# Kernel tuning notes

Hardware: AMD Instinct MI355X
Metric: run time of the kernel (lower is better)

Reference implementation:

```python
import jax, jax.numpy as jnp
import numpy as np

B, T, D, H = 4, 2048, 1024, 16
HD = D // H
EPS = 1e-5
NEG = 1e10


def setup_inputs() -> dict:
    key = jax.random.key(0)
    k1, k2, k3 = jax.random.split(key, 3)
    return {
        "target": jax.random.normal(k1, (B, T, D), dtype=jnp.float32),
        "w_qkv": jax.random.normal(k2, (D, 3 * D), dtype=jnp.float32) * 0.02,
        "w_proj": jax.random.normal(k3, (D, D), dtype=jnp.float32) * (0.02 / np.sqrt(24.0)),
        "b_proj": jnp.zeros((D,), dtype=jnp.float32),
        "ln_gamma": jnp.ones((D,), dtype=jnp.float32),
        "ln_beta": jnp.zeros((D,), dtype=jnp.float32),
    }


def reference(target, w_qkv, w_proj, b_proj, ln_gamma, ln_beta):
    b, t, d = target.shape
    resid = target
    qkv = target @ w_qkv                      # [B,T,3D]
    q, k, v = jnp.split(qkv, 3, axis=-1)
    # [B,H,T,hd]
    q = q.reshape(b, t, H, HD).transpose(0, 2, 1, 3)
    k = k.reshape(b, t, H, HD).transpose(0, 2, 1, 3)
    v = v.reshape(b, t, H, HD).transpose(0, 2, 1, 3)
    scores = jnp.einsum("bhqd,bhkd->bhqk", q, k) * (1.0 / np.sqrt(HD))
    causal = (jnp.arange(t)[:, None] >= jnp.arange(t)[None, :]).astype(scores.dtype)
    scores = scores * causal - (1.0 - causal) * NEG
    attn = jax.nn.softmax(scores, axis=-1)
    out = jnp.einsum("bhqk,bhkd->bhqd", attn, v)
    out = out.transpose(0, 2, 1, 3).reshape(b, t, d)
    proj = out @ w_proj + b_proj
    x = proj + resid
    mu = jnp.mean(x, axis=-1, keepdims=True)
    var = jnp.var(x, axis=-1, keepdims=True)
    return ((x - mu) * jax.lax.rsqrt(var + EPS)) * ln_gamma + ln_beta
```

## Files before the change

### kernel.cpp

```cpp
#include <hip/hip_runtime.h>
#include <hip/hip_bf16.h>

#define Bsz 4
#define Tseq 2048
#define Dmodel 1024
#define Hn 16
#define HD 64
#define EPS 1e-5f
#define QSCALE 0.18033688011112042f

typedef __attribute__((ext_vector_type(8))) short bf16x8;
typedef __attribute__((ext_vector_type(4))) float f32x4;
typedef __attribute__((ext_vector_type(4))) unsigned short us4;

typedef const __attribute__((address_space(1))) void* gas_t;
typedef __attribute__((address_space(3))) void* las_t;

__device__ __forceinline__ unsigned short f2bf(float x) {
    unsigned u = __builtin_bit_cast(unsigned, x);
    u += 0x7fffu + ((u >> 16) & 1u);
    return (unsigned short)(u >> 16);
}
__device__ __forceinline__ unsigned pack2bf_t(float a, float b) {
    return (__builtin_bit_cast(unsigned, a) >> 16)
         | (__builtin_bit_cast(unsigned, b) & 0xffff0000u);
}

__global__ void cast_bf16(const float* __restrict__ in, unsigned short* __restrict__ out) {
    int i = (blockIdx.x * 256 + threadIdx.x) * 4;
    float4 v = *(const float4*)(in + i);
    us4 o = { f2bf(v.x), f2bf(v.y), f2bf(v.z), f2bf(v.w) };
    *(us4*)(out + i) = o;
}

__global__ void transpose_cast(const float* __restrict__ in, unsigned short* __restrict__ out,
                               int K, int N) {
    __shared__ unsigned short t[32][33];
    int k0 = blockIdx.y * 32, n0 = blockIdx.x * 32;
    int tx = threadIdx.x, ty = threadIdx.y;
    #pragma unroll
    for (int i = 0; i < 32; i += 8)
        t[ty + i][tx] = f2bf(in[(size_t)(k0 + ty + i) * N + n0 + tx]);
    __syncthreads();
    #pragma unroll
    for (int i = 0; i < 32; i += 8)
        out[(size_t)(n0 + ty + i) * K + k0 + tx] = t[tx][ty + i];
}

template<bool OUT_BF16, bool SCALEQ>
__global__ __launch_bounds__(256)
void gemm_mfma(const unsigned short* __restrict__ A,
               const unsigned short* __restrict__ Bt,
               void* __restrict__ Cv, int M, int N, int K,
               const float* __restrict__ bias, const float* __restrict__ resid) {
    __shared__ unsigned short As[128 * 32];
    __shared__ unsigned short Bs[128 * 32];
    const int tid = threadIdx.x;
    const int w = tid >> 6, lane = tid & 63;
    const int l16 = lane & 15, quad = lane >> 4;
    const int m0 = blockIdx.y * 128, n0 = blockIdx.x * 128;

    f32x4 acc[4][4];
    #pragma unroll
    for (int i = 0; i < 4; ++i)
        #pragma unroll
        for (int j = 0; j < 4; ++j)
            acc[i][j] = f32x4{0.f, 0.f, 0.f, 0.f};

    const int lrow = lane >> 2, lcol = lane & 3;
    const unsigned short* ag = A  + (size_t)(m0 + w * 32 + lrow) * K + lcol * 8;
    const unsigned short* bg = Bt + (size_t)(n0 + w * 32 + lrow) * K + lcol * 8;
    unsigned short* al0 = As + (w * 32) * 32;
    unsigned short* al1 = As + (w * 32 + 16) * 32;
    unsigned short* bl0 = Bs + (w * 32) * 32;
    unsigned short* bl1 = Bs + (w * 32 + 16) * 32;
    const int am = (w >> 1) * 64, bn = (w & 1) * 64;

    for (int k0 = 0; k0 < K; k0 += 32) {
        __builtin_amdgcn_global_load_lds((gas_t)(ag + k0),          (las_t)al0, 16, 0, 0);
        __builtin_amdgcn_global_load_lds((gas_t)(ag + 16 * K + k0), (las_t)al1, 16, 0, 0);
        __builtin_amdgcn_global_load_lds((gas_t)(bg + k0),          (las_t)bl0, 16, 0, 0);
        __builtin_amdgcn_global_load_lds((gas_t)(bg + 16 * K + k0), (las_t)bl1, 16, 0, 0);
        __syncthreads();

        bf16x8 af[4], bf[4];
        #pragma unroll
        for (int i = 0; i < 4; ++i)
            af[i] = *(const bf16x8*)&As[(am + i * 16 + l16) * 32 + quad * 8];
        #pragma unroll
        for (int j = 0; j < 4; ++j)
            bf[j] = *(const bf16x8*)&Bs[(bn + j * 16 + l16) * 32 + quad * 8];
        #pragma unroll
        for (int i = 0; i < 4; ++i)
            #pragma unroll
            for (int j = 0; j < 4; ++j)
                acc[i][j] = __builtin_amdgcn_mfma_f32_16x16x32_bf16(af[i], bf[j], acc[i][j], 0, 0, 0);
        __syncthreads();
    }

    #pragma unroll
    for (int i = 0; i < 4; ++i) {
        #pragma unroll
        for (int j = 0; j < 4; ++j) {
            const int col = n0 + bn + j * 16 + l16;
            const float scale = (SCALEQ && col < Dmodel) ? QSCALE : 1.0f;
            #pragma unroll
            for (int r = 0; r < 4; ++r) {
                const int row = m0 + am + i * 16 + quad * 4 + r;
                if (OUT_BF16) {
                    ((unsigned short*)Cv)[(size_t)row * N + col] = f2bf(acc[i][j][r] * scale);
                } else {
                    float v = acc[i][j][r] + bias[col] + resid[(size_t)row * N + col];
                    ((float*)Cv)[(size_t)row * N + col] = v;
                }
            }
        }
    }
}

__global__ __launch_bounds__(256)
void flash_attn(const unsigned short* __restrict__ qkv, unsigned short* __restrict__ out) {
    const int x = blockIdx.x;
    const int qt_lo = x, qt_hi = (Tseq / 64 - 1) - x;
    const int bh = blockIdx.y;
    const int h = bh & (Hn - 1), b = bh >> 4;
    const int tid = threadIdx.x;
    const int wave = tid >> 6;
    const int lane = tid & 63;
    const int l16 = lane & 15;
    const int quad = lane >> 4;

    __shared__ unsigned short Ks[2][64 * 32];
    __shared__ unsigned short Vs[64 * 64];
    __shared__ unsigned short Ps[4][16 * 72];

    const unsigned short* qrow = qkv + ((size_t)(b * Tseq + wave * 16 + l16)) * 3072 + h * HD;
    const unsigned short* qhi = qrow + (size_t)qt_hi * 64 * 3072;
    const unsigned short* qlo = qrow + (size_t)qt_lo * 64 * 3072;
    bf16x8 qh0 = *(const bf16x8*)(qhi + quad * 8);
    bf16x8 qh1 = *(const bf16x8*)(qhi + 32 + quad * 8);
    bf16x8 ql0 = *(const bf16x8*)(qlo + quad * 8);
    bf16x8 ql1 = *(const bf16x8*)(qlo + 32 + quad * 8);

    float l_hi = 0.f, l_lo = 0.f;
    f32x4 ohi[4], olo[4];
    #pragma unroll
    for (int nt = 0; nt < 4; ++nt) {
        ohi[nt] = f32x4{0.f, 0.f, 0.f, 0.f};
        olo[nt] = f32x4{0.f, 0.f, 0.f, 0.f};
    }

    const unsigned short* kbase = qkv + (size_t)b * Tseq * 3072 + Dmodel + h * HD;
    const unsigned short* vbase = kbase + Dmodel;
    const unsigned short* kg = kbase + (size_t)(wave * 16 + (lane >> 2)) * 3072 + (lane & 3) * 8;
    unsigned short* kl0 = &Ks[0][wave * 16 * 32];
    unsigned short* kl1 = &Ks[1][wave * 16 * 32];
    const int vp = tid >> 3, vc = tid & 7;
    unsigned short* pw = Ps[wave];

    auto compute = [&](int q0t, const bf16x8& qf0, const bf16x8& qf1,
                       f32x4* oacc, float& l_part, bool diag, int k0g) {
        f32x4 st[4];
        #pragma unroll
        for (int nt = 0; nt < 4; ++nt) {
            f32x4 a = {0.f, 0.f, 0.f, 0.f};
            bf16x8 kf0 = *(const bf16x8*)&Ks[0][(nt * 16 + l16) * 32 + quad * 8];
            a = __builtin_amdgcn_mfma_f32_16x16x32_bf16(kf0, qf0, a, 0, 0, 0);
            bf16x8 kf1 = *(const bf16x8*)&Ks[1][(nt * 16 + l16) * 32 + quad * 8];
            a = __builtin_amdgcn_mfma_f32_16x16x32_bf16(kf1, qf1, a, 0, 0, 0);
            st[nt] = a;
        }
        if (diag) {
            const int qg = q0t + wave * 16 + l16;
            #pragma unroll
            for (int nt = 0; nt < 4; ++nt) {
                const int kgl = k0g + nt * 16 + quad * 4;
                #pragma unroll
                for (int r = 0; r < 4; ++r)
                    if (kgl + r > qg) st[nt][r] = -1e30f;
            }
        }
        float p[4][4];
        #pragma unroll
        for (int nt = 0; nt < 4; ++nt)
            #pragma unroll
            for (int r = 0; r < 4; ++r) {
                p[nt][r] = exp2f(st[nt][r]);
                l_part += p[nt][r];
            }
        #pragma unroll
        for (int nt = 0; nt < 4; ++nt) {
            unsigned* dst = (unsigned*)&pw[l16 * 72 + nt * 16 + quad * 4];
            dst[0] = pack2bf_t(p[nt][0], p[nt][1]);
            dst[1] = pack2bf_t(p[nt][2], p[nt][3]);
        }
        #pragma unroll
        for (int c = 0; c < 2; ++c) {
            bf16x8 pf = *(const bf16x8*)&pw[l16 * 72 + c * 32 + quad * 8];
            #pragma unroll
            for (int nt = 0; nt < 4; ++nt) {
                const int d = nt * 16 + l16;
                const int pc = (c * 4 + quad) ^ ((d + (d >> 3)) & 7);
                bf16x8 vf = *(const bf16x8*)&Vs[d * 64 + pc * 8];
                oacc[nt] = __builtin_amdgcn_mfma_f32_16x16x32_bf16(pf, vf, oacc[nt], 0, 0, 0);
            }
        }
    };

    for (int kt = 0; kt <= qt_hi; ++kt) {
        const size_t koff = (size_t)kt * 64 * 3072;
        __builtin_amdgcn_global_load_lds((gas_t)(kg + koff),      (las_t)kl0, 16, 0, 0);
        __builtin_amdgcn_global_load_lds((gas_t)(kg + koff + 32), (las_t)kl1, 16, 0, 0);
        {
            const unsigned short* vrow = vbase + koff + (size_t)(2 * vp) * 3072 + vc * 8;
            bf16x8 va = *(const bf16x8*)(vrow);
            bf16x8 vb = *(const bf16x8*)(vrow + 3072);
            const int kc = vp >> 2;
            const int kin = (2 * vp) & 7;
            #pragma unroll
            for (int j = 0; j < 8; ++j) {
                const int d = vc * 8 + j;
                const int pc = kc ^ ((d + (d >> 3)) & 7);
                unsigned pk = (unsigned)(unsigned short)va[j]
                            | ((unsigned)(unsigned short)vb[j] << 16);
                *(unsigned*)&Vs[d * 64 + pc * 8 + kin] = pk;
            }
        }
        __syncthreads();

        compute(qt_hi * 64, qh0, qh1, ohi, l_hi, kt == qt_hi, kt * 64);
        if (kt <= qt_lo)
            compute(qt_lo * 64, ql0, ql1, olo, l_lo, kt == qt_lo, kt * 64);
        __syncthreads();
    }

    auto epilogue = [&](int q0t, f32x4* oacc, float l_part) {
        l_part += __shfl_xor(l_part, 16, 64);
        l_part += __shfl_xor(l_part, 32, 64);
        float inv[4];
        #pragma unroll
        for (int r = 0; r < 4; ++r) {
            float lr = __shfl(l_part, quad * 4 + r, 64);
            inv[r] = __builtin_amdgcn_rcpf(lr);
        }
        unsigned short* obase =
            out + ((size_t)(b * Tseq + q0t + wave * 16)) * Dmodel + h * HD;
        #pragma unroll
        for (int nt = 0; nt < 4; ++nt) {
            #pragma unroll
            for (int r = 0; r < 4; ++r) {
                int row = quad * 4 + r;
                obase[(size_t)row * Dmodel + nt * 16 + l16] = f2bf(oacc[nt][r] * inv[r]);
            }
        }
    };
    epilogue(qt_hi * 64, ohi, l_hi);
    epilogue(qt_lo * 64, olo, l_lo);
}

__global__ void ln_kernel(float* __restrict__ x, const float* __restrict__ gamma,
                          const float* __restrict__ beta) {
    const int row = blockIdx.x;
    float* xr = x + (size_t)row * Dmodel;
    const int tid = threadIdx.x;
    __shared__ float rs[256], rs2[256];

    float4 v = *(const float4*)(xr + tid * 4);
    float s  = v.x + v.y + v.z + v.w;
    float s2 = v.x * v.x + v.y * v.y + v.z * v.z + v.w * v.w;
    rs[tid] = s; rs2[tid] = s2;
    __syncthreads();
    for (int off = 128; off; off >>= 1) {
        if (tid < off) { rs[tid] += rs[tid + off]; rs2[tid] += rs2[tid + off]; }
        __syncthreads();
    }
    const float mu  = rs[0] * (1.0f / Dmodel);
    const float var = rs2[0] * (1.0f / Dmodel) - mu * mu;
    const float rstd = rsqrtf(var + EPS);

    float4 g = *(const float4*)(gamma + tid * 4);
    float4 bt = *(const float4*)(beta + tid * 4);
    float4 o;
    o.x = (v.x - mu) * rstd * g.x + bt.x;
    o.y = (v.y - mu) * rstd * g.y + bt.y;
    o.z = (v.z - mu) * rstd * g.z + bt.z;
    o.w = (v.w - mu) * rstd * g.w + bt.w;
    *(float4*)(xr + tid * 4) = o;
}

extern "C" void kernel_launch(void* const* d_in, const int* in_sizes, int n_in,
                              void* d_out, int out_size, void* d_ws, size_t ws_size,
                              hipStream_t stream) {
    const float* target   = (const float*)d_in[0];
    const float* w_qkv    = (const float*)d_in[1];
    const float* w_proj   = (const float*)d_in[2];
    const float* b_proj   = (const float*)d_in[3];
    const float* ln_gamma = (const float*)d_in[4];
    const float* ln_beta  = (const float*)d_in[5];
    float* out = (float*)d_out;

    const int M = Bsz * Tseq;

    char* ws = (char*)d_ws;
    unsigned short* qkv_bf16 = (unsigned short*)(ws);
    unsigned short* attn_bf  = (unsigned short*)(ws + 48ull * 1024 * 1024);
    unsigned short* tgt_bf   = (unsigned short*)(ws + 64ull * 1024 * 1024);
    unsigned short* wqT      = (unsigned short*)(ws + 80ull * 1024 * 1024);
    unsigned short* wpT      = (unsigned short*)(ws + 86ull * 1024 * 1024);

    cast_bf16<<<dim3(M * Dmodel / 1024), 256, 0, stream>>>(target, tgt_bf);
    transpose_cast<<<dim3(3072 / 32, Dmodel / 32), dim3(32, 8), 0, stream>>>(
        w_qkv, wqT, Dmodel, 3072);
    transpose_cast<<<dim3(Dmodel / 32, Dmodel / 32), dim3(32, 8), 0, stream>>>(
        w_proj, wpT, Dmodel, Dmodel);

    gemm_mfma<true, true><<<dim3(3072 / 128, M / 128), 256, 0, stream>>>(
        tgt_bf, wqT, qkv_bf16, M, 3072, Dmodel, nullptr, nullptr);

    flash_attn<<<dim3(Tseq / 128, Bsz * Hn), 256, 0, stream>>>(qkv_bf16, attn_bf);

    gemm_mfma<false, false><<<dim3(Dmodel / 128, M / 128), 256, 0, stream>>>(
        attn_bf, wpT, out, M, Dmodel, Dmodel, b_proj, target);

    ln_kernel<<<dim3(M), 256, 0, stream>>>(out, ln_gamma, ln_beta);
}
```

Baseline: 322.2 us.

## Double-buffer V in LDS, load K fragments directly to registers, prefetch next V

Removes the K staging in shared memory. Each wave now loads its K MFMA fragments straight from global memory into registers, and every wave redundantly loads the full K tile. V is double-buffered in LDS: the next tile is loaded into registers during the current compute and written to the other buffer afterwards, which cuts one barrier per iteration. It also raises wave priority around the MFMA sections with s_setprio. The trade-off is four times more global/L2 traffic for K, uncoalesced 16-byte row loads, and higher register pressure from holding kf[8] plus the prefetched V.

```diff
diff --git a/kernel.cpp b/kernel.cpp
--- a/kernel.cpp
+++ b/kernel.cpp
@@ -130,8 +130,7 @@
     const int l16 = lane & 15;
     const int quad = lane >> 4;
 
-    __shared__ unsigned short Ks[2][64 * 32];
-    __shared__ unsigned short Vs[64 * 64];
+    __shared__ unsigned short Vs[2][64 * 64];
     __shared__ unsigned short Ps[4][16 * 72];
 
     const unsigned short* qrow = qkv + ((size_t)(b * Tseq + wave * 16 + l16)) * 3072 + h * HD;
@@ -152,22 +151,33 @@
 
     const unsigned short* kbase = qkv + (size_t)b * Tseq * 3072 + Dmodel + h * HD;
     const unsigned short* vbase = kbase + Dmodel;
-    const unsigned short* kg = kbase + (size_t)(wave * 16 + (lane >> 2)) * 3072 + (lane & 3) * 8;
-    unsigned short* kl0 = &Ks[0][wave * 16 * 32];
-    unsigned short* kl1 = &Ks[1][wave * 16 * 32];
+    const unsigned short* kfrag = kbase + (size_t)l16 * 3072 + quad * 8;
     const int vp = tid >> 3, vc = tid & 7;
+    const unsigned short* vsrc = vbase + (size_t)(2 * vp) * 3072 + vc * 8;
     unsigned short* pw = Ps[wave];
 
-    auto compute = [&](int q0t, const bf16x8& qf0, const bf16x8& qf1,
-                       f32x4* oacc, float& l_part, bool diag, int k0g) {
+    auto writeV = [&](int buf, const bf16x8& va, const bf16x8& vb) {
+        const int kc = vp >> 2;
+        const int kin = (2 * vp) & 7;
+        #pragma unroll
+        for (int j = 0; j < 8; ++j) {
+            const int d = vc * 8 + j;
+            const int pc = kc ^ ((d + (d >> 3)) & 7);
+            unsigned pk = (unsigned)(unsigned short)va[j]
+                        | ((unsigned)(unsigned short)vb[j] << 16);
+            *(unsigned*)&Vs[buf][d * 64 + pc * 8 + kin] = pk;
+        }
+    };
+
+    auto compute = [&](const bf16x8* kf, int q0t, const bf16x8& qf0, const bf16x8& qf1,
+                       f32x4* oacc, float& l_part, bool diag, int k0g, int vbuf) {
+        __builtin_amdgcn_s_setprio(1);
         f32x4 st[4];
         #pragma unroll
         for (int nt = 0; nt < 4; ++nt) {
             f32x4 a = {0.f, 0.f, 0.f, 0.f};
-            bf16x8 kf0 = *(const bf16x8*)&Ks[0][(nt * 16 + l16) * 32 + quad * 8];
-            a = __builtin_amdgcn_mfma_f32_16x16x32_bf16(kf0, qf0, a, 0, 0, 0);
-            bf16x8 kf1 = *(const bf16x8*)&Ks[1][(nt * 16 + l16) * 32 + quad * 8];
-            a = __builtin_amdgcn_mfma_f32_16x16x32_bf16(kf1, qf1, a, 0, 0, 0);
+            a = __builtin_amdgcn_mfma_f32_16x16x32_bf16(kf[2 * nt],     qf0, a, 0, 0, 0);
+            a = __builtin_amdgcn_mfma_f32_16x16x32_bf16(kf[2 * nt + 1], qf1, a, 0, 0, 0);
             st[nt] = a;
         }
         if (diag) {
@@ -201,37 +211,41 @@
             for (int nt = 0; nt < 4; ++nt) {
                 const int d = nt * 16 + l16;
                 const int pc = (c * 4 + quad) ^ ((d + (d >> 3)) & 7);
-                bf16x8 vf = *(const bf16x8*)&Vs[d * 64 + pc * 8];
+                bf16x8 vf = *(const bf16x8*)&Vs[vbuf][d * 64 + pc * 8];
                 oacc[nt] = __builtin_amdgcn_mfma_f32_16x16x32_bf16(pf, vf, oacc[nt], 0, 0, 0);
             }
         }
+        __builtin_amdgcn_s_setprio(0);
     };
 
+    bf16x8 va = *(const bf16x8*)(vsrc);
+    bf16x8 vb = *(const bf16x8*)(vsrc + 3072);
+    writeV(0, va, vb);
+    __syncthreads();
+
+    int cur = 0;
     for (int kt = 0; kt <= qt_hi; ++kt) {
         const size_t koff = (size_t)kt * 64 * 3072;
-        __builtin_amdgcn_global_load_lds((gas_t)(kg + koff),      (las_t)kl0, 16, 0, 0);
-        __builtin_amdgcn_global_load_lds((gas_t)(kg + koff + 32), (las_t)kl1, 16, 0, 0);
-        {
-            const unsigned short* vrow = vbase + koff + (size_t)(2 * vp) * 3072 + vc * 8;
-            bf16x8 va = *(const bf16x8*)(vrow);
-            bf16x8 vb = *(const bf16x8*)(vrow + 3072);
-            const int kc = vp >> 2;
-            const int kin = (2 * vp) & 7;
-            #pragma unroll
-            for (int j = 0; j < 8; ++j) {
-                const int d = vc * 8 + j;
-                const int pc = kc ^ ((d + (d >> 3)) & 7);
-                unsigned pk = (unsigned)(unsigned short)va[j]
-                            | ((unsigned)(unsigned short)vb[j] << 16);
-                *(unsigned*)&Vs[d * 64 + pc * 8 + kin] = pk;
-            }
-        }
+        if (kt < qt_hi) {
+            const unsigned short* vrow = vsrc + koff + (size_t)64 * 3072;
+            va = *(const bf16x8*)(vrow);
+            vb = *(const bf16x8*)(vrow + 3072);
+        }
+        bf16x8 kf[8];
+        #pragma unroll
+        for (int nt = 0; nt < 4; ++nt) {
+            const unsigned short* kr = kfrag + koff + (size_t)(nt * 16) * 3072;
+            kf[2 * nt]     = *(const bf16x8*)(kr);
+            kf[2 * nt + 1] = *(const bf16x8*)(kr + 32);
+        }
+
+        compute(kf, qt_hi * 64, qh0, qh1, ohi, l_hi, kt == qt_hi, kt * 64, cur);
+        if (kt <= qt_lo)
+            compute(kf, qt_lo * 64, ql0, ql1, olo, l_lo, kt == qt_lo, kt * 64, cur);
+
+        if (kt < qt_hi) writeV(cur ^ 1, va, vb);
         __syncthreads();
-
-        compute(qt_hi * 64, qh0, qh1, ohi, l_hi, kt == qt_hi, kt * 64);
-        if (kt <= qt_lo)
-            compute(qt_lo * 64, ql0, ql1, olo, l_lo, kt == qt_lo, kt * 64);
-        __syncthreads();
+        cur ^= 1;
     }
 
     auto epilogue = [&](int q0t, f32x4* oacc, float l_part) {
```

Measured after the change: 341.8 us. 1.06x slower.
